# Performance work log

Hardware: AMD Instinct MI355X
Metric: run time of the kernel (lower is better)

The kernel has to match this reference:

```python
import jax, jax.numpy as jnp
import numpy as np

N, E, D_IN, H, D_OUT = 50000, 1600000, 256, 128, 64


def setup_inputs() -> dict:
    key = jax.random.key(0)
    ks = jax.random.split(key, 8)
    x = jax.random.normal(ks[0], (N, D_IN), dtype=jnp.float32)
    edge_index = jax.random.randint(ks[1], (2, E), 0, N, dtype=jnp.int64)
    W1 = jax.random.normal(ks[2], (D_IN, H), dtype=jnp.float32) / np.float32(np.sqrt(D_IN))
    b1 = jnp.zeros((H,), jnp.float32)
    W2 = jax.random.normal(ks[3], (H, H), dtype=jnp.float32) / np.float32(np.sqrt(H))
    b2 = jnp.zeros((H,), jnp.float32)
    W3 = jax.random.normal(ks[4], (H, D_OUT), dtype=jnp.float32) / np.float32(np.sqrt(H))
    b3 = jnp.zeros((D_OUT,), jnp.float32)
    return {"x": x, "W1": W1, "b1": b1, "W2": W2, "b2": b2, "W3": W3, "b3": b3,
            "edge_index": edge_index}


def reference(x, W1, b1, W2, b2, W3, b3, edge_index):
    n = x.shape[0]
    # GCN: add self-loops, symmetric normalization D^{-1/2}(A+I)D^{-1/2}
    loop = jnp.arange(n, dtype=edge_index.dtype)
    src = jnp.concatenate([edge_index[0], loop])
    dst = jnp.concatenate([edge_index[1], loop])
    deg = jax.ops.segment_sum(jnp.ones_like(dst, x.dtype), dst, num_segments=n)
    dinv = jnp.where(deg > 0, jax.lax.rsqrt(deg), 0.0).astype(x.dtype)
    norm = dinv[src] * dinv[dst]  # [E+N]

    def gcn_layer(h, W, b):
        h = h @ W                                   # [N, F_out]
        msg = norm[:, None] * h[src]                # gather + scale, [E+N, F_out]
        return jax.ops.segment_sum(msg, dst, num_segments=n) + b

    h = jax.nn.relu(gcn_layer(x, W1, b1))
    h = jax.nn.relu(gcn_layer(h, W2, b2))
    return gcn_layer(h, W3, b3)
```

## Files before the change

kernel.cpp:

```cpp
#include <hip/hip_runtime.h>


constexpr int DIN = 256;
constexpr int HID = 128;
constexpr int DOUT = 64;

typedef unsigned short ushort_t;
typedef unsigned int uint_t;
typedef __attribute__((ext_vector_type(8))) short bf16x8;
typedef __attribute__((ext_vector_type(4))) float f32x4;

__device__ inline ushort_t f2bf(float f) {
  uint_t u = __float_as_uint(f);
  u += 0x7FFF + ((u >> 16) & 1);
  return (ushort_t)(u >> 16);
}
__device__ inline float bf2f(ushort_t b) {
  return __uint_as_float(((uint_t)b) << 16);
}


__device__ inline void wprep_one(const float* __restrict__ W, ushort_t* __restrict__ Bhi,
                                 ushort_t* __restrict__ Blo, int K, int F, int i) {
  int k = i / F, nn = i % F;
  int t = nn >> 4, s = k >> 5, q = (k >> 3) & 3, j = k & 7;
  int lane = q * 16 + (nn & 15);
  int KS = K >> 5;
  size_t idx = (((size_t)t * KS + s) * 64 + (size_t)lane) * 8 + j;
  float w = W[i];
  ushort_t h = f2bf(w);
  float r = w - bf2f(h);
  Bhi[idx] = h;
  Blo[idx] = f2bf(r);
}


__global__ __launch_bounds__(256) void initprep_kernel(
    int* __restrict__ c0, int* __restrict__ c1, int* __restrict__ c2,
    int* __restrict__ c3, int n, int iblocks,
    const float* __restrict__ W1, ushort_t* __restrict__ W1hi, ushort_t* __restrict__ W1lo,
    const float* __restrict__ W2, ushort_t* __restrict__ W2hi, ushort_t* __restrict__ W2lo,
    const float* __restrict__ W3, ushort_t* __restrict__ W3hi, ushort_t* __restrict__ W3lo) {
  if ((int)blockIdx.x < iblocks) {
    int i = blockIdx.x * 256 + threadIdx.x;
    if (i < n) { c0[i] = 1; c1[i] = 0; c2[i] = 0; c3[i] = 0; }
  } else {
    int idx = ((int)blockIdx.x - iblocks) * 256 + threadIdx.x;
    constexpr int S1 = DIN * HID;
    constexpr int S2 = S1 + HID * HID;
    constexpr int S3 = S2 + HID * DOUT;
    if (idx < S1) wprep_one(W1, W1hi, W1lo, DIN, HID, idx);
    else if (idx < S2) wprep_one(W2, W2hi, W2lo, HID, HID, idx - S1);
    else if (idx < S3) wprep_one(W3, W3hi, W3lo, HID, DOUT, idx - S2);
  }
}


template <int K, int F, bool SCALE>
__device__ inline void gemm_mfma_dev(const float* __restrict__ X,
    const ushort_t* __restrict__ Bhi, const ushort_t* __restrict__ Blo,
    const float* __restrict__ dinv, ushort_t* __restrict__ T, int n, int bid) {
  constexpr int NT = F / 16;
  constexpr int KS = K / 32;
  int wave = threadIdx.x >> 6;
  int lane = threadIdx.x & 63;
  int q = lane >> 4;
  int m = lane & 15;
  int arow = bid * 64 + wave * 16 + m;
  bool valid = arow < n;
  const float* xrow = X + (size_t)arow * K;

  f32x4 acc[NT];
#pragma unroll
  for (int t = 0; t < NT; ++t) acc[t] = (f32x4){0.f, 0.f, 0.f, 0.f};

  for (int s = 0; s < KS; ++s) {
    float av[8];
    if (valid) {
      float4 u0 = *(const float4*)(xrow + s * 32 + q * 8);
      float4 u1 = *(const float4*)(xrow + s * 32 + q * 8 + 4);
      av[0] = u0.x; av[1] = u0.y; av[2] = u0.z; av[3] = u0.w;
      av[4] = u1.x; av[5] = u1.y; av[6] = u1.z; av[7] = u1.w;
    } else {
#pragma unroll
      for (int j = 0; j < 8; ++j) av[j] = 0.f;
    }
    bf16x8 ahi, alo;
#pragma unroll
    for (int j = 0; j < 8; ++j) {
      ushort_t h = f2bf(av[j]);
      ahi[j] = (short)h;
      alo[j] = (short)f2bf(av[j] - bf2f(h));
    }
#pragma unroll
    for (int t = 0; t < NT; ++t) {
      size_t boff = (((size_t)t * KS + s) * 64 + (size_t)lane) * 8;
      bf16x8 bh = *(const bf16x8*)(Bhi + boff);
      bf16x8 bl = *(const bf16x8*)(Blo + boff);
      acc[t] = __builtin_amdgcn_mfma_f32_16x16x32_bf16(ahi, bh, acc[t], 0, 0, 0);
      acc[t] = __builtin_amdgcn_mfma_f32_16x16x32_bf16(alo, bh, acc[t], 0, 0, 0);
      acc[t] = __builtin_amdgcn_mfma_f32_16x16x32_bf16(ahi, bl, acc[t], 0, 0, 0);
    }
  }

  int orow_base = bid * 64 + wave * 16 + q * 4;
#pragma unroll
  for (int r = 0; r < 4; ++r) {
    int orow = orow_base + r;
    if (orow >= n) continue;
    float sc = SCALE ? dinv[orow] : 1.0f;
    ushort_t* trow = T + (size_t)orow * F + m;
#pragma unroll
    for (int t = 0; t < NT; ++t) trow[t * 16] = f2bf(sc * acc[t][r]);
  }
}

template <int K, int F>
__global__ __launch_bounds__(256) void gemm_mfma_kernel(const float* __restrict__ X,
    const ushort_t* __restrict__ Bhi, const ushort_t* __restrict__ Blo,
    const float* __restrict__ dinv, ushort_t* __restrict__ T, int n) {
  gemm_mfma_dev<K, F, true>(X, Bhi, Blo, dinv, T, n, blockIdx.x);
}


__global__ __launch_bounds__(256) void fusedA_kernel(
    const float* __restrict__ X, const ushort_t* __restrict__ Bhi,
    const ushort_t* __restrict__ Blo, ushort_t* __restrict__ T, int n, int gblocks,
    const int* __restrict__ dst, int* __restrict__ c0, int* __restrict__ c1,
    int* __restrict__ c2, int* __restrict__ c3, int* __restrict__ slot, int e) {
  if ((int)blockIdx.x < gblocks) {
    gemm_mfma_dev<DIN, HID, false>(X, Bhi, Blo, nullptr, T, n, blockIdx.x);
  } else {
    int i = ((int)blockIdx.x - gblocks) * 256 + threadIdx.x;
    if (i >= e) return;
    int d = dst[i];
    int k = i & 3;
    int s;
    if      (k == 0) s = atomicAdd(&c0[d], 1);
    else if (k == 1) s = atomicAdd(&c1[d], 1);
    else if (k == 2) s = atomicAdd(&c2[d], 1);
    else             s = atomicAdd(&c3[d], 1);
    slot[i] = s;
  }
}


__global__ __launch_bounds__(256) void scanA_kernel(const int* __restrict__ c0,
    const int* __restrict__ c1, const int* __restrict__ c2, const int* __restrict__ c3,
    int* __restrict__ blocksum, int n) {
  __shared__ int sums[256];
  int t = threadIdx.x;
  int base = blockIdx.x * 1024 + t * 4;
  int local = 0;
#pragma unroll
  for (int k = 0; k < 4; ++k) {
    int i = base + k;
    if (i < n) local += c0[i] + c1[i] + c2[i] + c3[i] - 1;
  }
  sums[t] = local;
  __syncthreads();
  for (int off = 128; off > 0; off >>= 1) {
    if (t < off) sums[t] += sums[t + off];
    __syncthreads();
  }
  if (t == 0) blocksum[blockIdx.x] = sums[0];
}

__global__ __launch_bounds__(64) void scanB_kernel(int* __restrict__ blocksum, int nb) {
  int lane = threadIdx.x;
  int carry = 0;
  for (int base = 0; base < nb; base += 64) {
    int i = base + lane;
    int orig = (i < nb) ? blocksum[i] : 0;
    int v = orig;
#pragma unroll
    for (int off = 1; off < 64; off <<= 1) {
      int u = __shfl_up(v, off, 64);
      if (lane >= off) v += u;
    }
    int total = __shfl(v, 63, 64);
    if (i < nb) blocksum[i] = carry + v - orig;
    carry += total;
  }
}

__global__ __launch_bounds__(256) void scanC_kernel(const int* __restrict__ c0,
    const int* __restrict__ c1, const int* __restrict__ c2, const int* __restrict__ c3,
    const int* __restrict__ blocksum, int* __restrict__ row_start, int* __restrict__ deg,
    float* __restrict__ dinv, int4* __restrict__ sub, int n) {
  __shared__ int sums[256];
  int t = threadIdx.x;
  int base = blockIdx.x * 1024 + t * 4;
  int d[4], k0[4], k1[4], k2[4];
  int local = 0;
#pragma unroll
  for (int k = 0; k < 4; ++k) {
    int i = base + k;
    if (i < n) {
      k0[k] = c0[i]; k1[k] = c1[i]; k2[k] = c2[i];
      d[k] = k0[k] + k1[k] + k2[k] + c3[i];
      local += d[k] - 1;
    } else { d[k] = 1; k0[k] = 1; k1[k] = 0; k2[k] = 0; }
  }
  sums[t] = local;
  __syncthreads();
  for (int off = 1; off < 256; off <<= 1) {
    int v = (t >= off) ? sums[t - off] : 0;
    __syncthreads();
    sums[t] += v;
    __syncthreads();
  }
  int run = blocksum[blockIdx.x] + sums[t] - local;
#pragma unroll
  for (int k = 0; k < 4; ++k) {
    int i = base + k;
    if (i < n) {
      row_start[i] = run;
      deg[i] = d[k];
      dinv[i] = rsqrtf((float)d[k]);
      int4 sb;
      sb.x = run - 1;
      sb.y = run + (k0[k] - 1);
      sb.z = sb.y + k1[k];
      sb.w = sb.z + k2[k];
      sub[i] = sb;
      run += d[k] - 1;
    }
  }
}


__global__ __launch_bounds__(256) void fusedB_kernel(
    const int* __restrict__ src, const int* __restrict__ dst,
    const int* __restrict__ slot, const int4* __restrict__ sub,
    int* __restrict__ col, int e, int fblocks,
    ushort_t* __restrict__ T, const float* __restrict__ dinv, int n) {
  if ((int)blockIdx.x < fblocks) {
    int i = blockIdx.x * 256 + threadIdx.x;
    if (i >= e) return;
    int d = dst[i];
    int k = i & 3;
    int4 sb = sub[d];
    int base = (k == 0) ? sb.x : (k == 1) ? sb.y : (k == 2) ? sb.z : sb.w;
    col[base + slot[i]] = src[i];
  } else {
    int idx = ((int)blockIdx.x - fblocks) * 256 + threadIdx.x;
    int total = n * (HID / 8);
    if (idx >= total) return;
    int row = idx >> 4;
    float sc = dinv[row];
    uint4* p = (uint4*)T + idx;
    uint4 v = *p;
    uint_t w[4] = {v.x, v.y, v.z, v.w};
#pragma unroll
    for (int j = 0; j < 4; ++j) {
      float lo = sc * bf2f((ushort_t)(w[j] & 0xFFFF));
      float hi = sc * bf2f((ushort_t)(w[j] >> 16));
      w[j] = (uint_t)f2bf(lo) | ((uint_t)f2bf(hi) << 16);
    }
    v.x = w[0]; v.y = w[1]; v.z = w[2]; v.w = w[3];
    *p = v;
  }
}


template <int F, bool RELU>
__global__ __launch_bounds__(256) void spmm_kernel(const ushort_t* __restrict__ t,
    const int* __restrict__ row_start, const int* __restrict__ deg,
    const int* __restrict__ col, const float* __restrict__ dinv,
    const float* __restrict__ bias, float* __restrict__ out, int n) {
  int gw = (int)((blockIdx.x * 256u + threadIdx.x) >> 6);
  int lane = threadIdx.x & 63;
  int n0 = gw * 2;
  int n1 = n0 + 1;
  if (n0 >= n) return;
  bool h1 = (n1 < n);
  int rs0 = row_start[n0], e0 = deg[n0] - 1;
  int rs1 = h1 ? row_start[n1] : 0, e1 = h1 ? (deg[n1] - 1) : 0;
  float di0 = dinv[n0];
  float di1 = h1 ? dinv[n1] : 0.f;

  if constexpr (F == 128) {
    uint_t s0 = ((const uint_t*)(t + (size_t)n0 * F))[lane];
    float ax0 = bf2f((ushort_t)(s0 & 0xFFFF)), ay0 = bf2f((ushort_t)(s0 >> 16));
    float ax1 = 0.f, ay1 = 0.f;
    if (h1) {
      uint_t s1 = ((const uint_t*)(t + (size_t)n1 * F))[lane];
      ax1 = bf2f((ushort_t)(s1 & 0xFFFF)); ay1 = bf2f((ushort_t)(s1 >> 16));
    }
    int p0 = rs0, q0 = rs0 + e0;
    int p1 = rs1, q1 = rs1 + e1;
    while (p0 + 4 <= q0 && p1 + 4 <= q1) {
      int c[8];
      uint_t v[8];
#pragma unroll
      for (int j = 0; j < 4; ++j) { c[j] = col[p0 + j]; c[4 + j] = col[p1 + j]; }
#pragma unroll
      for (int j = 0; j < 8; ++j) v[j] = ((const uint_t*)(t + (size_t)c[j] * F))[lane];
#pragma unroll
      for (int j = 0; j < 4; ++j) {
        ax0 += bf2f((ushort_t)(v[j] & 0xFFFF));
        ay0 += bf2f((ushort_t)(v[j] >> 16));
        ax1 += bf2f((ushort_t)(v[4 + j] & 0xFFFF));
        ay1 += bf2f((ushort_t)(v[4 + j] >> 16));
      }
      p0 += 4; p1 += 4;
    }
    for (; p0 + 4 <= q0; p0 += 4) {
      int c[4]; uint_t v[4];
#pragma unroll
      for (int j = 0; j < 4; ++j) c[j] = col[p0 + j];
#pragma unroll
      for (int j = 0; j < 4; ++j) v[j] = ((const uint_t*)(t + (size_t)c[j] * F))[lane];
#pragma unroll
      for (int j = 0; j < 4; ++j) {
        ax0 += bf2f((ushort_t)(v[j] & 0xFFFF)); ay0 += bf2f((ushort_t)(v[j] >> 16));
      }
    }
    for (; p0 < q0; ++p0) {
      uint_t v = ((const uint_t*)(t + (size_t)col[p0] * F))[lane];
      ax0 += bf2f((ushort_t)(v & 0xFFFF)); ay0 += bf2f((ushort_t)(v >> 16));
    }
    for (; p1 + 4 <= q1; p1 += 4) {
      int c[4]; uint_t v[4];
#pragma unroll
      for (int j = 0; j < 4; ++j) c[j] = col[p1 + j];
#pragma unroll
      for (int j = 0; j < 4; ++j) v[j] = ((const uint_t*)(t + (size_t)c[j] * F))[lane];
#pragma unroll
      for (int j = 0; j < 4; ++j) {
        ax1 += bf2f((ushort_t)(v[j] & 0xFFFF)); ay1 += bf2f((ushort_t)(v[j] >> 16));
      }
    }
    for (; p1 < q1; ++p1) {
      uint_t v = ((const uint_t*)(t + (size_t)col[p1] * F))[lane];
      ax1 += bf2f((ushort_t)(v & 0xFFFF)); ay1 += bf2f((ushort_t)(v >> 16));
    }
    float bx = bias[2 * lane], by = bias[2 * lane + 1];
    ax0 = fmaf(di0, ax0, bx); ay0 = fmaf(di0, ay0, by);
    if constexpr (RELU) { ax0 = fmaxf(ax0, 0.f); ay0 = fmaxf(ay0, 0.f); }
    float2 o0; o0.x = ax0; o0.y = ay0;
    ((float2*)(out + (size_t)n0 * F))[lane] = o0;
    if (h1) {
      ax1 = fmaf(di1, ax1, bx); ay1 = fmaf(di1, ay1, by);
      if constexpr (RELU) { ax1 = fmaxf(ax1, 0.f); ay1 = fmaxf(ay1, 0.f); }
      float2 o1; o1.x = ax1; o1.y = ay1;
      ((float2*)(out + (size_t)n1 * F))[lane] = o1;
    }
  } else {
    float a0 = bf2f(t[(size_t)n0 * F + lane]);
    float a1 = h1 ? bf2f(t[(size_t)n1 * F + lane]) : 0.f;
    int p0 = rs0, q0 = rs0 + e0;
    int p1 = rs1, q1 = rs1 + e1;
    while (p0 + 4 <= q0 && p1 + 4 <= q1) {
      int c[8];
      ushort_t v[8];
#pragma unroll
      for (int j = 0; j < 4; ++j) { c[j] = col[p0 + j]; c[4 + j] = col[p1 + j]; }
#pragma unroll
      for (int j = 0; j < 8; ++j) v[j] = t[(size_t)c[j] * F + lane];
#pragma unroll
      for (int j = 0; j < 4; ++j) { a0 += bf2f(v[j]); a1 += bf2f(v[4 + j]); }
      p0 += 4; p1 += 4;
    }
    for (; p0 + 4 <= q0; p0 += 4) {
      int c[4]; ushort_t v[4];
#pragma unroll
      for (int j = 0; j < 4; ++j) c[j] = col[p0 + j];
#pragma unroll
      for (int j = 0; j < 4; ++j) v[j] = t[(size_t)c[j] * F + lane];
#pragma unroll
      for (int j = 0; j < 4; ++j) a0 += bf2f(v[j]);
    }
    for (; p0 < q0; ++p0) a0 += bf2f(t[(size_t)col[p0] * F + lane]);
    for (; p1 + 4 <= q1; p1 += 4) {
      int c[4]; ushort_t v[4];
#pragma unroll
      for (int j = 0; j < 4; ++j) c[j] = col[p1 + j];
#pragma unroll
      for (int j = 0; j < 4; ++j) v[j] = t[(size_t)c[j] * F + lane];
#pragma unroll
      for (int j = 0; j < 4; ++j) a1 += bf2f(v[j]);
    }
    for (; p1 < q1; ++p1) a1 += bf2f(t[(size_t)col[p1] * F + lane]);
    float b = bias[lane];
    a0 = fmaf(di0, a0, b);
    if constexpr (RELU) a0 = fmaxf(a0, 0.f);
    out[(size_t)n0 * F + lane] = a0;
    if (h1) {
      a1 = fmaf(di1, a1, b);
      if constexpr (RELU) a1 = fmaxf(a1, 0.f);
      out[(size_t)n1 * F + lane] = a1;
    }
  }
}


extern "C" void kernel_launch(void* const* d_in, const int* in_sizes, int n_in,
                              void* d_out, int out_size, void* d_ws, size_t ws_size,
                              hipStream_t stream) {
  const float* x  = (const float*)d_in[0];
  const float* W1 = (const float*)d_in[1];
  const float* b1 = (const float*)d_in[2];
  const float* W2 = (const float*)d_in[3];
  const float* b2 = (const float*)d_in[4];
  const float* W3 = (const float*)d_in[5];
  const float* b3 = (const float*)d_in[6];
  const int* ei   = (const int*)d_in[7];

  int n = in_sizes[0] / DIN;
  int e = in_sizes[7] / 2;
  const int* src = ei;
  const int* dst = ei + e;

  char* ws = (char*)d_ws;
  size_t off = 0;
  auto alloc = [&](size_t bytes) -> void* {
    off = (off + 255) & ~(size_t)255;
    void* p = ws + off;
    off += bytes;
    return p;
  };
  int nscan = (n + 1023) / 1024;
  int*      c0        = (int*)alloc((size_t)n * 4);
  int*      c1        = (int*)alloc((size_t)n * 4);
  int*      c2        = (int*)alloc((size_t)n * 4);
  int*      c3        = (int*)alloc((size_t)n * 4);
  int*      deg       = (int*)alloc((size_t)n * 4);
  float*    dinv      = (float*)alloc((size_t)n * 4);
  int*      row_start = (int*)alloc((size_t)n * 4);
  int4*     sub       = (int4*)alloc((size_t)n * 16);
  int*      blocksum  = (int*)alloc((size_t)nscan * 4);
  int*      slot      = (int*)alloc((size_t)e * 4);
  int*      col       = (int*)alloc((size_t)e * 4);
  ushort_t* T         = (ushort_t*)alloc((size_t)n * HID * 2);
  float*    Hf        = (float*)alloc((size_t)n * HID * 4);
  ushort_t* W1hi      = (ushort_t*)alloc((size_t)DIN * HID * 2);
  ushort_t* W1lo      = (ushort_t*)alloc((size_t)DIN * HID * 2);
  ushort_t* W2hi      = (ushort_t*)alloc((size_t)HID * HID * 2);
  ushort_t* W2lo      = (ushort_t*)alloc((size_t)HID * HID * 2);
  ushort_t* W3hi      = (ushort_t*)alloc((size_t)HID * DOUT * 2);
  ushort_t* W3lo      = (ushort_t*)alloc((size_t)HID * DOUT * 2);
  (void)ws_size;

  int nb256 = (n + 255) / 256;
  int eb256 = (e + 255) / 256;
  int gemm_blocks = (n + 63) / 64;
  int nwaves = (n + 1) / 2;
  int spmm_blocks = (nwaves + 3) / 4;
  constexpr int WPREP_TOTAL = DIN * HID + HID * HID + HID * DOUT;
  int wblocks = (WPREP_TOTAL + 255) / 256;
  int sblocks = (n * (HID / 8) + 255) / 256;

  initprep_kernel<<<nb256 + wblocks, 256, 0, stream>>>(
      c0, c1, c2, c3, n, nb256,
      W1, W1hi, W1lo, W2, W2hi, W2lo, W3, W3hi, W3lo);
  fusedA_kernel<<<gemm_blocks + eb256, 256, 0, stream>>>(
      x, W1hi, W1lo, T, n, gemm_blocks,
      dst, c0, c1, c2, c3, slot, e);
  scanA_kernel<<<nscan, 256, 0, stream>>>(c0, c1, c2, c3, blocksum, n);
  scanB_kernel<<<1, 64, 0, stream>>>(blocksum, nscan);
  scanC_kernel<<<nscan, 256, 0, stream>>>(c0, c1, c2, c3, blocksum, row_start, deg, dinv, sub, n);
  fusedB_kernel<<<eb256 + sblocks, 256, 0, stream>>>(
      src, dst, slot, sub, col, e, eb256, T, dinv, n);

  spmm_kernel<HID, true><<<spmm_blocks, 256, 0, stream>>>(T, row_start, deg, col, dinv, b1, Hf, n);
  gemm_mfma_kernel<HID, HID><<<gemm_blocks, 256, 0, stream>>>(Hf, W2hi, W2lo, dinv, T, n);
  spmm_kernel<HID, true><<<spmm_blocks, 256, 0, stream>>>(T, row_start, deg, col, dinv, b2, Hf, n);
  gemm_mfma_kernel<HID, DOUT><<<gemm_blocks, 256, 0, stream>>>(Hf, W3hi, W3lo, dinv, T, n);
  spmm_kernel<DOUT, false><<<spmm_blocks, 256, 0, stream>>>(T, row_start, deg, col, dinv, b3, (float*)d_out, n);
}
```

Before: 402.0 us.

## Pad per-node atomic counters to separate cache lines and vectorize edge counting

The four sub-counter arrays are merged into one padded array in which every (node, sub-bin) counter sits on its own 64-byte line, so atomics from different sub-bins no longer contend on shared lines. Each thread in the counting phase now handles four edges through int4 loads and stores. scanA additionally writes the compacted counts to a deg4 array, which scanC reads instead of the strided counters. The cost is a much larger counter buffer (n*256 bytes) and more scattered init and scan reads.

Result: slower. 421.2 us (+4.8%).

```diff
diff --git a/kernel.cpp b/kernel.cpp
--- a/kernel.cpp
+++ b/kernel.cpp
@@ -18,6 +18,8 @@
 __device__ inline float bf2f(ushort_t b) {
   return __uint_as_float(((uint_t)b) << 16);
 }
+
+__device__ inline int cidx(int d, int k) { return ((d << 2) | k) << 4; }
 
 
 __device__ inline void wprep_one(const float* __restrict__ W, ushort_t* __restrict__ Bhi,
@@ -36,14 +38,18 @@
 
 
 __global__ __launch_bounds__(256) void initprep_kernel(
-    int* __restrict__ c0, int* __restrict__ c1, int* __restrict__ c2,
-    int* __restrict__ c3, int n, int iblocks,
+    int* __restrict__ cnt, int n, int iblocks,
     const float* __restrict__ W1, ushort_t* __restrict__ W1hi, ushort_t* __restrict__ W1lo,
     const float* __restrict__ W2, ushort_t* __restrict__ W2hi, ushort_t* __restrict__ W2lo,
     const float* __restrict__ W3, ushort_t* __restrict__ W3hi, ushort_t* __restrict__ W3lo) {
   if ((int)blockIdx.x < iblocks) {
     int i = blockIdx.x * 256 + threadIdx.x;
-    if (i < n) { c0[i] = 1; c1[i] = 0; c2[i] = 0; c3[i] = 0; }
+    if (i < n) {
+      cnt[cidx(i, 0)] = 1;
+      cnt[cidx(i, 1)] = 0;
+      cnt[cidx(i, 2)] = 0;
+      cnt[cidx(i, 3)] = 0;
+    }
   } else {
     int idx = ((int)blockIdx.x - iblocks) * 256 + threadIdx.x;
     constexpr int S1 = DIN * HID;
@@ -126,28 +132,34 @@
 __global__ __launch_bounds__(256) void fusedA_kernel(
     const float* __restrict__ X, const ushort_t* __restrict__ Bhi,
     const ushort_t* __restrict__ Blo, ushort_t* __restrict__ T, int n, int gblocks,
-    const int* __restrict__ dst, int* __restrict__ c0, int* __restrict__ c1,
-    int* __restrict__ c2, int* __restrict__ c3, int* __restrict__ slot, int e) {
+    const int* __restrict__ dst, int* __restrict__ cnt,
+    int* __restrict__ slot, int e) {
   if ((int)blockIdx.x < gblocks) {
     gemm_mfma_dev<DIN, HID, false>(X, Bhi, Blo, nullptr, T, n, blockIdx.x);
   } else {
-    int i = ((int)blockIdx.x - gblocks) * 256 + threadIdx.x;
-    if (i >= e) return;
-    int d = dst[i];
-    int k = i & 3;
-    int s;
-    if      (k == 0) s = atomicAdd(&c0[d], 1);
-    else if (k == 1) s = atomicAdd(&c1[d], 1);
-    else if (k == 2) s = atomicAdd(&c2[d], 1);
-    else             s = atomicAdd(&c3[d], 1);
-    slot[i] = s;
-  }
-}
-
-
-__global__ __launch_bounds__(256) void scanA_kernel(const int* __restrict__ c0,
-    const int* __restrict__ c1, const int* __restrict__ c2, const int* __restrict__ c3,
-    int* __restrict__ blocksum, int n) {
+    int i0 = ((((int)blockIdx.x - gblocks) * 256 + (int)threadIdx.x)) * 4;
+    if (i0 >= e) return;
+    if (i0 + 4 <= e) {
+      int4 d4 = *(const int4*)(dst + i0);
+      int s0 = atomicAdd(&cnt[cidx(d4.x, 0)], 1);
+      int s1 = atomicAdd(&cnt[cidx(d4.y, 1)], 1);
+      int s2 = atomicAdd(&cnt[cidx(d4.z, 2)], 1);
+      int s3 = atomicAdd(&cnt[cidx(d4.w, 3)], 1);
+      int4 s4;
+      s4.x = s0; s4.y = s1; s4.z = s2; s4.w = s3;
+      *(int4*)(slot + i0) = s4;
+    } else {
+      for (int i = i0; i < e; ++i) {
+        int d = dst[i];
+        slot[i] = atomicAdd(&cnt[cidx(d, i & 3)], 1);
+      }
+    }
+  }
+}
+
+
+__global__ __launch_bounds__(256) void scanA_kernel(const int* __restrict__ cnt,
+    int4* __restrict__ deg4, int* __restrict__ blocksum, int n) {
   __shared__ int sums[256];
   int t = threadIdx.x;
   int base = blockIdx.x * 1024 + t * 4;
@@ -155,7 +167,16 @@
 #pragma unroll
   for (int k = 0; k < 4; ++k) {
     int i = base + k;
-    if (i < n) local += c0[i] + c1[i] + c2[i] + c3[i] - 1;
+    if (i < n) {
+      int k0 = cnt[cidx(i, 0)];
+      int k1 = cnt[cidx(i, 1)];
+      int k2 = cnt[cidx(i, 2)];
+      int k3 = cnt[cidx(i, 3)];
+      int4 v;
+      v.x = k0; v.y = k1; v.z = k2; v.w = k3;
+      deg4[i] = v;
+      local += k0 + k1 + k2 + k3 - 1;
+    }
   }
   sums[t] = local;
   __syncthreads();
@@ -184,8 +205,7 @@
   }
 }
 
-__global__ __launch_bounds__(256) void scanC_kernel(const int* __restrict__ c0,
-    const int* __restrict__ c1, const int* __restrict__ c2, const int* __restrict__ c3,
+__global__ __launch_bounds__(256) void scanC_kernel(const int4* __restrict__ deg4,
     const int* __restrict__ blocksum, int* __restrict__ row_start, int* __restrict__ deg,
     float* __restrict__ dinv, int4* __restrict__ sub, int n) {
   __shared__ int sums[256];
@@ -197,8 +217,9 @@
   for (int k = 0; k < 4; ++k) {
     int i = base + k;
     if (i < n) {
-      k0[k] = c0[i]; k1[k] = c1[i]; k2[k] = c2[i];
-      d[k] = k0[k] + k1[k] + k2[k] + c3[i];
+      int4 v = deg4[i];
+      k0[k] = v.x; k1[k] = v.y; k2[k] = v.z;
+      d[k] = v.x + v.y + v.z + v.w;
       local += d[k] - 1;
     } else { d[k] = 1; k0[k] = 1; k1[k] = 0; k2[k] = 0; }
   }
@@ -422,10 +443,8 @@
     return p;
   };
   int nscan = (n + 1023) / 1024;
-  int*      c0        = (int*)alloc((size_t)n * 4);
-  int*      c1        = (int*)alloc((size_t)n * 4);
-  int*      c2        = (int*)alloc((size_t)n * 4);
-  int*      c3        = (int*)alloc((size_t)n * 4);
+  int*      cnt       = (int*)alloc((size_t)n * 4 * 64);
+  int4*     deg4      = (int4*)alloc((size_t)n * 16);
   int*      deg       = (int*)alloc((size_t)n * 4);
   float*    dinv      = (float*)alloc((size_t)n * 4);
   int*      row_start = (int*)alloc((size_t)n * 4);
@@ -445,6 +464,7 @@
 
   int nb256 = (n + 255) / 256;
   int eb256 = (e + 255) / 256;
+  int db1024 = (e + 1023) / 1024;
   int gemm_blocks = (n + 63) / 64;
   int nwaves = (n + 1) / 2;
   int spmm_blocks = (nwaves + 3) / 4;
@@ -453,14 +473,14 @@
   int sblocks = (n * (HID / 8) + 255) / 256;
 
   initprep_kernel<<<nb256 + wblocks, 256, 0, stream>>>(
-      c0, c1, c2, c3, n, nb256,
+      cnt, n, nb256,
       W1, W1hi, W1lo, W2, W2hi, W2lo, W3, W3hi, W3lo);
-  fusedA_kernel<<<gemm_blocks + eb256, 256, 0, stream>>>(
+  fusedA_kernel<<<gemm_blocks + db1024, 256, 0, stream>>>(
       x, W1hi, W1lo, T, n, gemm_blocks,
-      dst, c0, c1, c2, c3, slot, e);
-  scanA_kernel<<<nscan, 256, 0, stream>>>(c0, c1, c2, c3, blocksum, n);
+      dst, cnt, slot, e);
+  scanA_kernel<<<nscan, 256, 0, stream>>>(cnt, deg4, blocksum, n);
   scanB_kernel<<<1, 64, 0, stream>>>(blocksum, nscan);
-  scanC_kernel<<<nscan, 256, 0, stream>>>(c0, c1, c2, c3, blocksum, row_start, deg, dinv, sub, n);
+  scanC_kernel<<<nscan, 256, 0, stream>>>(deg4, blocksum, row_start, deg, dinv, sub, n);
   fusedB_kernel<<<eb256 + sblocks, 256, 0, stream>>>(
       src, dst, slot, sub, col, e, eb256, T, dinv, n);
 
```

## Build CSR via bucketed binning with LDS atomics instead of global per-node counters

Applied to the files above, without the earlier changes.

Replaces the global-atomic degree counting, three-pass scan and scatter with a two-level bucket sort: per-block LDS histograms over 64-node buckets, a single-block bucket scan, a binning pass packing (dst,src) into 32-bit words, and a per-bucket kernel that builds row_start, deg, dinv and col using shared-memory atomics. The separate pass that scales T by dinv is removed; instead the first SpMM multiplies each gathered neighbour by dinv[col] in the inner loop. This aims to cut global atomic contention and kernel launches. The 16-bit packing assumes node ids fit in 16 bits, which is false for N=50000 with dst<<16 (dst fits, but src up to 50000 fits 16 bits; dst<<16 fits in 32). MAXB limits node count to 65536, and the extra dinv gather adds loads to layer-1 SpMM.

Result: faster. 354.5 us (-11.8%).

```diff
diff --git a/kernel.cpp b/kernel.cpp
--- a/kernel.cpp
+++ b/kernel.cpp
@@ -4,6 +4,9 @@
 constexpr int DIN = 256;
 constexpr int HID = 128;
 constexpr int DOUT = 64;
+constexpr int MAXB = 1024;
+constexpr int BSH = 6;
+constexpr int EPB = 8192;
 
 typedef unsigned short ushort_t;
 typedef unsigned int uint_t;
@@ -36,14 +39,13 @@
 
 
 __global__ __launch_bounds__(256) void initprep_kernel(
-    int* __restrict__ c0, int* __restrict__ c1, int* __restrict__ c2,
-    int* __restrict__ c3, int n, int iblocks,
+    int* __restrict__ bucket_total, int iblocks,
     const float* __restrict__ W1, ushort_t* __restrict__ W1hi, ushort_t* __restrict__ W1lo,
     const float* __restrict__ W2, ushort_t* __restrict__ W2hi, ushort_t* __restrict__ W2lo,
     const float* __restrict__ W3, ushort_t* __restrict__ W3hi, ushort_t* __restrict__ W3lo) {
   if ((int)blockIdx.x < iblocks) {
     int i = blockIdx.x * 256 + threadIdx.x;
-    if (i < n) { c0[i] = 1; c1[i] = 0; c2[i] = 0; c3[i] = 0; }
+    if (i < MAXB) bucket_total[i] = 0;
   } else {
     int idx = ((int)blockIdx.x - iblocks) * 256 + threadIdx.x;
     constexpr int S1 = DIN * HID;
@@ -53,6 +55,54 @@
     else if (idx < S2) wprep_one(W2, W2hi, W2lo, HID, HID, idx - S1);
     else if (idx < S3) wprep_one(W3, W3hi, W3lo, HID, DOUT, idx - S2);
   }
+}
+
+
+__global__ __launch_bounds__(256) void bin_kernel(const int* __restrict__ dst, int e,
+    int nbuckets, int* __restrict__ bucket_total, int* __restrict__ block_base) {
+  __shared__ int h[MAXB];
+  int tid = threadIdx.x;
+  for (int i = tid; i < nbuckets; i += 256) h[i] = 0;
+  __syncthreads();
+  int base = blockIdx.x * EPB;
+  int end = min(base + EPB, e);
+  for (int i = base + tid; i < end; i += 256) atomicAdd(&h[dst[i] >> BSH], 1);
+  __syncthreads();
+  for (int i = tid; i < nbuckets; i += 256) {
+    int v = h[i];
+    if (v) block_base[(size_t)blockIdx.x * nbuckets + i] = atomicAdd(&bucket_total[i], v);
+  }
+}
+
+
+__global__ __launch_bounds__(256) void scan_buckets_kernel(const int* __restrict__ total,
+    int* __restrict__ base, int nb) {
+  __shared__ int sums[256];
+  int t = threadIdx.x;
+  int a[4];
+  int ls = 0;
+#pragma unroll
+  for (int k = 0; k < 4; ++k) {
+    int idx = t * 4 + k;
+    a[k] = (idx < nb) ? total[idx] : 0;
+    ls += a[k];
+  }
+  sums[t] = ls;
+  __syncthreads();
+  for (int off = 1; off < 256; off <<= 1) {
+    int u = (t >= off) ? sums[t - off] : 0;
+    __syncthreads();
+    sums[t] += u;
+    __syncthreads();
+  }
+  int run = sums[t] - ls;
+#pragma unroll
+  for (int k = 0; k < 4; ++k) {
+    int idx = t * 4 + k;
+    if (idx < nb) base[idx] = run;
+    run += a[k];
+  }
+  if (t == 255) base[nb] = sums[255];
 }
 
 
@@ -123,148 +173,82 @@
 }
 
 
-__global__ __launch_bounds__(256) void fusedA_kernel(
+__global__ __launch_bounds__(256) void fusedA2_kernel(
     const float* __restrict__ X, const ushort_t* __restrict__ Bhi,
     const ushort_t* __restrict__ Blo, ushort_t* __restrict__ T, int n, int gblocks,
-    const int* __restrict__ dst, int* __restrict__ c0, int* __restrict__ c1,
-    int* __restrict__ c2, int* __restrict__ c3, int* __restrict__ slot, int e) {
+    const int* __restrict__ src, const int* __restrict__ dst,
+    const int* __restrict__ bucket_base, const int* __restrict__ block_base,
+    uint_t* __restrict__ binned, int e, int nbuckets) {
   if ((int)blockIdx.x < gblocks) {
     gemm_mfma_dev<DIN, HID, false>(X, Bhi, Blo, nullptr, T, n, blockIdx.x);
   } else {
-    int i = ((int)blockIdx.x - gblocks) * 256 + threadIdx.x;
-    if (i >= e) return;
-    int d = dst[i];
-    int k = i & 3;
-    int s;
-    if      (k == 0) s = atomicAdd(&c0[d], 1);
-    else if (k == 1) s = atomicAdd(&c1[d], 1);
-    else if (k == 2) s = atomicAdd(&c2[d], 1);
-    else             s = atomicAdd(&c3[d], 1);
-    slot[i] = s;
-  }
-}
-
-
-__global__ __launch_bounds__(256) void scanA_kernel(const int* __restrict__ c0,
-    const int* __restrict__ c1, const int* __restrict__ c2, const int* __restrict__ c3,
-    int* __restrict__ blocksum, int n) {
-  __shared__ int sums[256];
-  int t = threadIdx.x;
-  int base = blockIdx.x * 1024 + t * 4;
-  int local = 0;
-#pragma unroll
-  for (int k = 0; k < 4; ++k) {
-    int i = base + k;
-    if (i < n) local += c0[i] + c1[i] + c2[i] + c3[i] - 1;
-  }
-  sums[t] = local;
-  __syncthreads();
-  for (int off = 128; off > 0; off >>= 1) {
-    if (t < off) sums[t] += sums[t + off];
+    __shared__ int rkh[MAXB];
+    __shared__ int cbase[MAXB];
+    int tid = threadIdx.x;
+    int blk = (int)blockIdx.x - gblocks;
+    for (int i = tid; i < nbuckets; i += 256) {
+      rkh[i] = 0;
+      cbase[i] = bucket_base[i] + block_base[(size_t)blk * nbuckets + i];
+    }
     __syncthreads();
-  }
-  if (t == 0) blocksum[blockIdx.x] = sums[0];
-}
-
-__global__ __launch_bounds__(64) void scanB_kernel(int* __restrict__ blocksum, int nb) {
-  int lane = threadIdx.x;
-  int carry = 0;
-  for (int base = 0; base < nb; base += 64) {
-    int i = base + lane;
-    int orig = (i < nb) ? blocksum[i] : 0;
-    int v = orig;
+    int base = blk * EPB;
+    int end = min(base + EPB, e);
+    for (int i = base + tid; i < end; i += 256) {
+      int d = dst[i];
+      int s = src[i];
+      int b = d >> BSH;
+      int r = atomicAdd(&rkh[b], 1);
+      binned[cbase[b] + r] = ((uint_t)d << 16) | (uint_t)s;
+    }
+  }
+}
+
+
+__global__ __launch_bounds__(256) void csr_kernel(const uint_t* __restrict__ binned,
+    const int* __restrict__ bucket_base, int n, int* __restrict__ row_start,
+    int* __restrict__ deg, float* __restrict__ dinv, int* __restrict__ col) {
+  __shared__ int cnt[64];
+  __shared__ int rk[64];
+  __shared__ int rs[64];
+  __shared__ int ebs[2];
+  int tid = threadIdx.x;
+  int b = blockIdx.x;
+  int node0 = b << BSH;
+  if (tid < 64) { cnt[tid] = 0; rk[tid] = 0; }
+  if (tid == 0) { ebs[0] = bucket_base[b]; ebs[1] = bucket_base[b + 1]; }
+  __syncthreads();
+  int ebase = ebs[0];
+  int esz = ebs[1] - ebase;
+  for (int i = tid; i < esz; i += 256)
+    atomicAdd(&cnt[(int)(binned[ebase + i] >> 16) - node0], 1);
+  __syncthreads();
+  if (tid < 64) {
+    int v = cnt[tid];
+    int inc = v;
 #pragma unroll
     for (int off = 1; off < 64; off <<= 1) {
-      int u = __shfl_up(v, off, 64);
-      if (lane >= off) v += u;
-    }
-    int total = __shfl(v, 63, 64);
-    if (i < nb) blocksum[i] = carry + v - orig;
-    carry += total;
-  }
-}
-
-__global__ __launch_bounds__(256) void scanC_kernel(const int* __restrict__ c0,
-    const int* __restrict__ c1, const int* __restrict__ c2, const int* __restrict__ c3,
-    const int* __restrict__ blocksum, int* __restrict__ row_start, int* __restrict__ deg,
-    float* __restrict__ dinv, int4* __restrict__ sub, int n) {
-  __shared__ int sums[256];
-  int t = threadIdx.x;
-  int base = blockIdx.x * 1024 + t * 4;
-  int d[4], k0[4], k1[4], k2[4];
-  int local = 0;
-#pragma unroll
-  for (int k = 0; k < 4; ++k) {
-    int i = base + k;
-    if (i < n) {
-      k0[k] = c0[i]; k1[k] = c1[i]; k2[k] = c2[i];
-      d[k] = k0[k] + k1[k] + k2[k] + c3[i];
-      local += d[k] - 1;
-    } else { d[k] = 1; k0[k] = 1; k1[k] = 0; k2[k] = 0; }
-  }
-  sums[t] = local;
-  __syncthreads();
-  for (int off = 1; off < 256; off <<= 1) {
-    int v = (t >= off) ? sums[t - off] : 0;
-    __syncthreads();
-    sums[t] += v;
-    __syncthreads();
-  }
-  int run = blocksum[blockIdx.x] + sums[t] - local;
-#pragma unroll
-  for (int k = 0; k < 4; ++k) {
-    int i = base + k;
-    if (i < n) {
-      row_start[i] = run;
-      deg[i] = d[k];
-      dinv[i] = rsqrtf((float)d[k]);
-      int4 sb;
-      sb.x = run - 1;
-      sb.y = run + (k0[k] - 1);
-      sb.z = sb.y + k1[k];
-      sb.w = sb.z + k2[k];
-      sub[i] = sb;
-      run += d[k] - 1;
-    }
-  }
-}
-
-
-__global__ __launch_bounds__(256) void fusedB_kernel(
-    const int* __restrict__ src, const int* __restrict__ dst,
-    const int* __restrict__ slot, const int4* __restrict__ sub,
-    int* __restrict__ col, int e, int fblocks,
-    ushort_t* __restrict__ T, const float* __restrict__ dinv, int n) {
-  if ((int)blockIdx.x < fblocks) {
-    int i = blockIdx.x * 256 + threadIdx.x;
-    if (i >= e) return;
-    int d = dst[i];
-    int k = i & 3;
-    int4 sb = sub[d];
-    int base = (k == 0) ? sb.x : (k == 1) ? sb.y : (k == 2) ? sb.z : sb.w;
-    col[base + slot[i]] = src[i];
-  } else {
-    int idx = ((int)blockIdx.x - fblocks) * 256 + threadIdx.x;
-    int total = n * (HID / 8);
-    if (idx >= total) return;
-    int row = idx >> 4;
-    float sc = dinv[row];
-    uint4* p = (uint4*)T + idx;
-    uint4 v = *p;
-    uint_t w[4] = {v.x, v.y, v.z, v.w};
-#pragma unroll
-    for (int j = 0; j < 4; ++j) {
-      float lo = sc * bf2f((ushort_t)(w[j] & 0xFFFF));
-      float hi = sc * bf2f((ushort_t)(w[j] >> 16));
-      w[j] = (uint_t)f2bf(lo) | ((uint_t)f2bf(hi) << 16);
-    }
-    v.x = w[0]; v.y = w[1]; v.z = w[2]; v.w = w[3];
-    *p = v;
-  }
-}
-
-
-template <int F, bool RELU>
+      int u = __shfl_up(inc, off, 64);
+      if (tid >= off) inc += u;
+    }
+    rs[tid] = inc - v;
+    int node = node0 + tid;
+    if (node < n) {
+      deg[node] = v + 1;
+      dinv[node] = rsqrtf((float)(v + 1));
+      row_start[node] = ebase + (inc - v);
+    }
+  }
+  __syncthreads();
+  for (int i = tid; i < esz; i += 256) {
+    uint_t p = binned[ebase + i];
+    int l = (int)(p >> 16) - node0;
+    int r = atomicAdd(&rk[l], 1);
+    col[ebase + rs[l] + r] = (int)(p & 0xFFFFu);
+  }
+}
+
+
+template <int F, bool RELU, bool GD>
 __global__ __launch_bounds__(256) void spmm_kernel(const ushort_t* __restrict__ t,
     const int* __restrict__ row_start, const int* __restrict__ deg,
     const int* __restrict__ col, const float* __restrict__ dinv,
@@ -283,58 +267,101 @@
   if constexpr (F == 128) {
     uint_t s0 = ((const uint_t*)(t + (size_t)n0 * F))[lane];
     float ax0 = bf2f((ushort_t)(s0 & 0xFFFF)), ay0 = bf2f((ushort_t)(s0 >> 16));
+    if constexpr (GD) { ax0 *= di0; ay0 *= di0; }
     float ax1 = 0.f, ay1 = 0.f;
     if (h1) {
       uint_t s1 = ((const uint_t*)(t + (size_t)n1 * F))[lane];
       ax1 = bf2f((ushort_t)(s1 & 0xFFFF)); ay1 = bf2f((ushort_t)(s1 >> 16));
+      if constexpr (GD) { ax1 *= di1; ay1 *= di1; }
     }
     int p0 = rs0, q0 = rs0 + e0;
     int p1 = rs1, q1 = rs1 + e1;
     while (p0 + 4 <= q0 && p1 + 4 <= q1) {
       int c[8];
       uint_t v[8];
+      float dc[8];
 #pragma unroll
       for (int j = 0; j < 4; ++j) { c[j] = col[p0 + j]; c[4 + j] = col[p1 + j]; }
 #pragma unroll
-      for (int j = 0; j < 8; ++j) v[j] = ((const uint_t*)(t + (size_t)c[j] * F))[lane];
+      for (int j = 0; j < 8; ++j) {
+        v[j] = ((const uint_t*)(t + (size_t)c[j] * F))[lane];
+        if constexpr (GD) dc[j] = dinv[c[j]];
+      }
 #pragma unroll
       for (int j = 0; j < 4; ++j) {
-        ax0 += bf2f((ushort_t)(v[j] & 0xFFFF));
-        ay0 += bf2f((ushort_t)(v[j] >> 16));
-        ax1 += bf2f((ushort_t)(v[4 + j] & 0xFFFF));
-        ay1 += bf2f((ushort_t)(v[4 + j] >> 16));
+        if constexpr (GD) {
+          ax0 = fmaf(dc[j], bf2f((ushort_t)(v[j] & 0xFFFF)), ax0);
+          ay0 = fmaf(dc[j], bf2f((ushort_t)(v[j] >> 16)), ay0);
+          ax1 = fmaf(dc[4 + j], bf2f((ushort_t)(v[4 + j] & 0xFFFF)), ax1);
+          ay1 = fmaf(dc[4 + j], bf2f((ushort_t)(v[4 + j] >> 16)), ay1);
+        } else {
+          ax0 += bf2f((ushort_t)(v[j] & 0xFFFF));
+          ay0 += bf2f((ushort_t)(v[j] >> 16));
+          ax1 += bf2f((ushort_t)(v[4 + j] & 0xFFFF));
+          ay1 += bf2f((ushort_t)(v[4 + j] >> 16));
+        }
       }
       p0 += 4; p1 += 4;
     }
     for (; p0 + 4 <= q0; p0 += 4) {
-      int c[4]; uint_t v[4];
+      int c[4]; uint_t v[4]; float dc[4];
 #pragma unroll
       for (int j = 0; j < 4; ++j) c[j] = col[p0 + j];
 #pragma unroll
-      for (int j = 0; j < 4; ++j) v[j] = ((const uint_t*)(t + (size_t)c[j] * F))[lane];
-#pragma unroll
       for (int j = 0; j < 4; ++j) {
-        ax0 += bf2f((ushort_t)(v[j] & 0xFFFF)); ay0 += bf2f((ushort_t)(v[j] >> 16));
+        v[j] = ((const uint_t*)(t + (size_t)c[j] * F))[lane];
+        if constexpr (GD) dc[j] = dinv[c[j]];
+      }
+#pragma unroll
+      for (int j = 0; j < 4; ++j) {
+        if constexpr (GD) {
+          ax0 = fmaf(dc[j], bf2f((ushort_t)(v[j] & 0xFFFF)), ax0);
+          ay0 = fmaf(dc[j], bf2f((ushort_t)(v[j] >> 16)), ay0);
+        } else {
+          ax0 += bf2f((ushort_t)(v[j] & 0xFFFF)); ay0 += bf2f((ushort_t)(v[j] >> 16));
+        }
       }
     }
     for (; p0 < q0; ++p0) {
-      uint_t v = ((const uint_t*)(t + (size_t)col[p0] * F))[lane];
-      ax0 += bf2f((ushort_t)(v & 0xFFFF)); ay0 += bf2f((ushort_t)(v >> 16));
+      int c = col[p0];
+      uint_t v = ((const uint_t*)(t + (size_t)c * F))[lane];
+      float d = GD ? dinv[c] : 1.f;
+      if constexpr (GD) {
+        ax0 = fmaf(d, bf2f((ushort_t)(v & 0xFFFF)), ax0);
+        ay0 = fmaf(d, bf2f((ushort_t)(v >> 16)), ay0);
+      } else {
+        ax0 += bf2f((ushort_t)(v & 0xFFFF)); ay0 += bf2f((ushort_t)(v >> 16));
+      }
     }
     for (; p1 + 4 <= q1; p1 += 4) {
-      int c[4]; uint_t v[4];
+      int c[4]; uint_t v[4]; float dc[4];
 #pragma unroll
       for (int j = 0; j < 4; ++j) c[j] = col[p1 + j];
 #pragma unroll
-      for (int j = 0; j < 4; ++j) v[j] = ((const uint_t*)(t + (size_t)c[j] * F))[lane];
-#pragma unroll
       for (int j = 0; j < 4; ++j) {
-        ax1 += bf2f((ushort_t)(v[j] & 0xFFFF)); ay1 += bf2f((ushort_t)(v[j] >> 16));
+        v[j] = ((const uint_t*)(t + (size_t)c[j] * F))[lane];
+        if constexpr (GD) dc[j] = dinv[c[j]];
+      }
+#pragma unroll
+      for (int j = 0; j < 4; ++j) {
+        if constexpr (GD) {
+          ax1 = fmaf(dc[j], bf2f((ushort_t)(v[j] & 0xFFFF)), ax1);
+          ay1 = fmaf(dc[j], bf2f((ushort_t)(v[j] >> 16)), ay1);
+        } else {
+          ax1 += bf2f((ushort_t)(v[j] & 0xFFFF)); ay1 += bf2f((ushort_t)(v[j] >> 16));
+        }
       }
     }
     for (; p1 < q1; ++p1) {
-      uint_t v = ((const uint_t*)(t + (size_t)col[p1] * F))[lane];
-      ax1 += bf2f((ushort_t)(v & 0xFFFF)); ay1 += bf2f((ushort_t)(v >> 16));
+      int c = col[p1];
+      uint_t v = ((const uint_t*)(t + (size_t)c * F))[lane];
+      float d = GD ? dinv[c] : 1.f;
+      if constexpr (GD) {
+        ax1 = fmaf(d, bf2f((ushort_t)(v & 0xFFFF)), ax1);
+        ay1 = fmaf(d, bf2f((ushort_t)(v >> 16)), ay1);
+      } else {
+        ax1 += bf2f((ushort_t)(v & 0xFFFF)); ay1 += bf2f((ushort_t)(v >> 16));
+      }
     }
     float bx = bias[2 * lane], by = bias[2 * lane + 1];
     ax0 = fmaf(di0, ax0, bx); ay0 = fmaf(di0, ay0, by);
@@ -421,52 +448,47 @@
     off += bytes;
     return p;
   };
-  int nscan = (n + 1023) / 1024;
-  int*      c0        = (int*)alloc((size_t)n * 4);
-  int*      c1        = (int*)alloc((size_t)n * 4);
-  int*      c2        = (int*)alloc((size_t)n * 4);
-  int*      c3        = (int*)alloc((size_t)n * 4);
-  int*      deg       = (int*)alloc((size_t)n * 4);
-  float*    dinv      = (float*)alloc((size_t)n * 4);
-  int*      row_start = (int*)alloc((size_t)n * 4);
-  int4*     sub       = (int4*)alloc((size_t)n * 16);
-  int*      blocksum  = (int*)alloc((size_t)nscan * 4);
-  int*      slot      = (int*)alloc((size_t)e * 4);
-  int*      col       = (int*)alloc((size_t)e * 4);
-  ushort_t* T         = (ushort_t*)alloc((size_t)n * HID * 2);
-  float*    Hf        = (float*)alloc((size_t)n * HID * 4);
-  ushort_t* W1hi      = (ushort_t*)alloc((size_t)DIN * HID * 2);
-  ushort_t* W1lo      = (ushort_t*)alloc((size_t)DIN * HID * 2);
-  ushort_t* W2hi      = (ushort_t*)alloc((size_t)HID * HID * 2);
-  ushort_t* W2lo      = (ushort_t*)alloc((size_t)HID * HID * 2);
-  ushort_t* W3hi      = (ushort_t*)alloc((size_t)HID * DOUT * 2);
-  ushort_t* W3lo      = (ushort_t*)alloc((size_t)HID * DOUT * 2);
+  int nbuckets = (n + 63) >> BSH;
+  int nbin = (e + EPB - 1) / EPB;
+
+  int*      bucket_total = (int*)alloc((size_t)MAXB * 4);
+  int*      bucket_base  = (int*)alloc((size_t)(MAXB + 1) * 4);
+  int*      block_base   = (int*)alloc((size_t)nbin * nbuckets * 4);
+  uint_t*   binned       = (uint_t*)alloc((size_t)e * 4);
+  int*      deg          = (int*)alloc((size_t)n * 4);
+  float*    dinv         = (float*)alloc((size_t)n * 4);
+  int*      row_start    = (int*)alloc((size_t)n * 4);
+  int*      col          = (int*)alloc((size_t)e * 4);
+  ushort_t* T            = (ushort_t*)alloc((size_t)n * HID * 2);
+  float*    Hf           = (float*)alloc((size_t)n * HID * 4);
+  ushort_t* W1hi         = (ushort_t*)alloc((size_t)DIN * HID * 2);
+  ushort_t* W1lo         = (ushort_t*)alloc((size_t)DIN * HID * 2);
+  ushort_t* W2hi         = (ushort_t*)alloc((size_t)HID * HID * 2);
+  ushort_t* W2lo         = (ushort_t*)alloc((size_t)HID * HID * 2);
+  ushort_t* W3hi         = (ushort_t*)alloc((size_t)HID * DOUT * 2);
+  ushort_t* W3lo         = (ushort_t*)alloc((size_t)HID * DOUT * 2);
   (void)ws_size;
 
-  int nb256 = (n + 255) / 256;
-  int eb256 = (e + 255) / 256;
   int gemm_blocks = (n + 63) / 64;
   int nwaves = (n + 1) / 2;
   int spmm_blocks = (nwaves + 3) / 4;
   constexpr int WPREP_TOTAL = DIN * HID + HID * HID + HID * DOUT;
   int wblocks = (WPREP_TOTAL + 255) / 256;
-  int sblocks = (n * (HID / 8) + 255) / 256;
-
-  initprep_kernel<<<nb256 + wblocks, 256, 0, stream>>>(
-      c0, c1, c2, c3, n, nb256,
+  int iblocks = MAXB / 256;
+
+  initprep_kernel<<<iblocks + wblocks, 256, 0, stream>>>(
+      bucket_total, iblocks,
       W1, W1hi, W1lo, W2, W2hi, W2lo, W3, W3hi, W3lo);
-  fusedA_kernel<<<gemm_blocks + eb256, 256, 0, stream>>>(
+  bin_kernel<<<nbin, 256, 0, stream>>>(dst, e, nbuckets, bucket_total, block_base);
+  scan_buckets_kernel<<<1, 256, 0, stream>>>(bucket_total, bucket_base, nbuckets);
+  fusedA2_kernel<<<gemm_blocks + nbin, 256, 0, stream>>>(
       x, W1hi, W1lo, T, n, gemm_blocks,
-      dst, c0, c1, c2, c3, slot, e);
-  scanA_kernel<<<nscan, 256, 0, stream>>>(c0, c1, c2, c3, blocksum, n);
-  scanB_kernel<<<1, 64, 0, stream>>>(blocksum, nscan);
-  scanC_kernel<<<nscan, 256, 0, stream>>>(c0, c1, c2, c3, blocksum, row_start, deg, dinv, sub, n);
-  fusedB_kernel<<<eb256 + sblocks, 256, 0, stream>>>(
-      src, dst, slot, sub, col, e, eb256, T, dinv, n);
-
-  spmm_kernel<HID, true><<<spmm_blocks, 256, 0, stream>>>(T, row_start, deg, col, dinv, b1, Hf, n);
+      src, dst, bucket_base, block_base, binned, e, nbuckets);
+  csr_kernel<<<nbuckets, 256, 0, stream>>>(binned, bucket_base, n, row_start, deg, dinv, col);
+
+  spmm_kernel<HID, true, true><<<spmm_blocks, 256, 0, stream>>>(T, row_start, deg, col, dinv, b1, Hf, n);
   gemm_mfma_kernel<HID, HID><<<gemm_blocks, 256, 0, stream>>>(Hf, W2hi, W2lo, dinv, T, n);
-  spmm_kernel<HID, true><<<spmm_blocks, 256, 0, stream>>>(T, row_start, deg, col, dinv, b2, Hf, n);
+  spmm_kernel<HID, true, false><<<spmm_blocks, 256, 0, stream>>>(T, row_start, deg, col, dinv, b2, Hf, n);
   gemm_mfma_kernel<HID, DOUT><<<gemm_blocks, 256, 0, stream>>>(Hf, W3hi, W3lo, dinv, T, n);
-  spmm_kernel<DOUT, false><<<spmm_blocks, 256, 0, stream>>>(T, row_start, deg, col, dinv, b3, (float*)d_out, n);
-}
+  spmm_kernel<DOUT, false, false><<<spmm_blocks, 256, 0, stream>>>(T, row_start, deg, col, dinv, b3, (float*)d_out, n);
+}
```
